# Kernel tuning notes

Measured on AMD Instinct MI355X. Metric: run time of the kernel, lower is better.

## Reference

```python
import jax, jax.numpy as jnp
import numpy as np

N_NODES = 100000
N_REL = 4
N_EDGES = 600000
D = 128


def setup_inputs() -> dict:
    key = jax.random.key(0)
    k1, k2, k3 = jax.random.split(key, 3)
    edges = jax.random.randint(k1, (N_REL, 2, N_EDGES), 0, N_NODES, dtype=jnp.int32)
    X = jax.random.normal(k2, (N_NODES, D), dtype=jnp.float32)
    # one weight matrix per relation (GraphConv weight=True, bias=False)
    W = jax.random.normal(k3, (N_REL, D, D), dtype=jnp.float32) * (1.0 / np.sqrt(D))
    return {"edges": edges, "X": X, "W": W}


def _graphconv_both(src, dst, X, W):
    # DGL GraphConv, norm='both', no bias/activation, allow_zero_in_degree.
    ones = jnp.ones((src.shape[0],), dtype=X.dtype)
    deg_out = jax.ops.segment_sum(ones, src, num_segments=N_NODES).clip(1.0)
    deg_in = jax.ops.segment_sum(ones, dst, num_segments=N_NODES).clip(1.0)
    h = X * jax.lax.rsqrt(deg_out)[:, None]          # [N, D] src-normalized
    agg = jax.ops.segment_sum(h[src], dst, num_segments=N_NODES)  # SpMM: [N, D]
    agg = agg * jax.lax.rsqrt(deg_in)[:, None]
    return agg @ W                                   # dense transform [N, D]


def reference(edges, X, W):
    # sum of per-relation GraphConv outputs (stack(...).sum(0))
    Z = jnp.zeros((N_NODES, W.shape[-1]), dtype=X.dtype)
    for r in range(N_REL):  # small fixed relation count
        Z = Z + _graphconv_both(edges[r, 0], edges[r, 1], X, W[r])
    return Z
```

## Files before the change

kernel.cpp:

```cpp
#include <hip/hip_runtime.h>
#include <hip/hip_bf16.h>

constexpr int N_NODES = 100000;
constexpr int N_REL   = 4;
constexpr int N_EDGES = 600000;
constexpr int MAXDEG  = 32;
constexpr int D       = 128;
constexpr int KTOT    = N_REL * D;
constexpr int M_PAD   = 100096;

constexpr int NB   = 128;
constexpr int BW   = 784;
constexpr int NKEY = N_REL * NB;
constexpr int CAP  = 5632;
constexpr int EPB  = 2048;
constexpr int TOT_E   = N_REL * N_EDGES;
constexpr int P1_BLKS = (TOT_E + EPB - 1) / EPB;
constexpr int XC_BLKS = (N_NODES * D / 4) / 256;
constexpr int WC_BLKS = (N_REL * D * D) / 256;

typedef __attribute__((ext_vector_type(8))) short bf16x8;
typedef __attribute__((ext_vector_type(4))) float f32x4;

static __device__ __forceinline__ unsigned short f2bf(float f) {
    union { float f; unsigned int u; } v; v.f = f;
    unsigned int r = (v.u + 0x7fffu + ((v.u >> 16) & 1u)) >> 16;
    return (unsigned short)r;
}

__global__ __launch_bounds__(256) void pass1(const int* __restrict__ edges,
                                             int* __restrict__ gcur,
                                             unsigned* __restrict__ bktd,
                                             unsigned* __restrict__ bkts,
                                             const float* __restrict__ X,
                                             unsigned short* __restrict__ Xb,
                                             const float* __restrict__ W,
                                             unsigned short* __restrict__ Wt) {
    int b = blockIdx.x;
    if (b < P1_BLKS) {
        __shared__ int hd[NKEY], hs[NKEY], bd[NKEY], bs[NKEY];
        int tid = threadIdx.x;
        for (int k = tid; k < NKEY; k += 256) { hd[k] = 0; hs[k] = 0; }
        __syncthreads();

        int e0 = b * EPB;
        int src[8], dst[8], kd[8], ks[8];
#pragma unroll
        for (int k = 0; k < 8; k++) {
            int t = e0 + k * 256 + tid;
            kd[k] = -1; ks[k] = -1; src[k] = 0; dst[k] = 0;
            if (t < TOT_E) {
                int r = t / N_EDGES;
                int e = t - r * N_EDGES;
                src[k] = edges[(size_t)(r * 2)     * N_EDGES + e];
                dst[k] = edges[(size_t)(r * 2 + 1) * N_EDGES + e];
                kd[k] = r * NB + dst[k] / BW;
                ks[k] = r * NB + src[k] / BW;
                atomicAdd(&hd[kd[k]], 1);
                atomicAdd(&hs[ks[k]], 1);
            }
        }
        __syncthreads();
        for (int k = tid; k < NKEY; k += 256) {
            int c = hd[k];
            bd[k] = c ? atomicAdd(&gcur[k * 16], c) : 0;
            hd[k] = 0;
            c = hs[k];
            bs[k] = c ? atomicAdd(&gcur[(NKEY + k) * 16], c) : 0;
            hs[k] = 0;
        }
        __syncthreads();
#pragma unroll
        for (int k = 0; k < 8; k++) {
            if (kd[k] >= 0) {
                int dstloc = dst[k] - (kd[k] - (kd[k] >> 7) * NB) * BW;
                int p = bd[kd[k]] + atomicAdd(&hd[kd[k]], 1);
                if (p < CAP) bktd[(size_t)kd[k] * CAP + p] = (unsigned)src[k] | ((unsigned)dstloc << 17);
                p = bs[ks[k]] + atomicAdd(&hs[ks[k]], 1);
                if (p < CAP) bkts[(size_t)ks[k] * CAP + p] = (unsigned)src[k];
            }
        }
    } else if (b < P1_BLKS + XC_BLKS) {
        int t = (b - P1_BLKS) * 256 + threadIdx.x;
        float4 v = ((const float4*)X)[t];
        union { unsigned short u[4]; uint2 d; } o;
        o.u[0] = f2bf(v.x); o.u[1] = f2bf(v.y); o.u[2] = f2bf(v.z); o.u[3] = f2bf(v.w);
        ((uint2*)Xb)[t] = o.d;
    } else {
        int t = (b - P1_BLKS - XC_BLKS) * 256 + threadIdx.x;
        int r = t >> 14;
        int k = (t >> 7) & 127;
        int n = t & 127;
        Wt[(size_t)n * KTOT + r * D + k] = f2bf(W[t]);
    }
}

__global__ __launch_bounds__(1024) void pass2a(const int* __restrict__ gcur,
                                               const unsigned* __restrict__ bkts,
                                               float* __restrict__ routf) {
    __shared__ int cur[BW];
    int b = blockIdx.x, tid = threadIdx.x;
    if (tid < BW) cur[tid] = 0;
    __syncthreads();
    int r = b >> 7;
    int node0 = (b & 127) * BW;
    int cnt = min(gcur[(NKEY + b) * 16], CAP);
    for (int i = tid; i < cnt; i += 1024)
        atomicAdd(&cur[(int)bkts[(size_t)b * CAP + i] - node0], 1);
    __syncthreads();
    int nN = min(BW, N_NODES - node0);
    if (tid < nN) {
        int c = cur[tid];
        routf[r * N_NODES + node0 + tid] = rsqrtf((float)(c < 1 ? 1 : c));
    }
}

__global__ __launch_bounds__(1024) void pass2b(const int* __restrict__ gcur,
                                               const unsigned* __restrict__ bktd,
                                               const float* __restrict__ routf,
                                               uint2* __restrict__ esrcc,
                                               int* __restrict__ indeg) {
    __shared__ int cur[BW];
    int b = blockIdx.x, tid = threadIdx.x;
    if (tid < BW) cur[tid] = 0;
    __syncthreads();
    int r = b >> 7;
    int node0 = (b & 127) * BW;
    int cnt = min(gcur[b * 16], CAP);
    for (int i = tid; i < cnt; i += 1024) {
        unsigned rec = bktd[(size_t)b * CAP + i];
        int s      = (int)(rec & 0x1FFFFu);
        int dstloc = (int)(rec >> 17);
        int pos = atomicAdd(&cur[dstloc], 1);
        if (pos < MAXDEG) {
            union { float f; unsigned u; } c; c.f = routf[r * N_NODES + s];
            esrcc[((size_t)r * N_NODES + node0 + dstloc) * MAXDEG + pos] = make_uint2((unsigned)s, c.u);
        }
    }
    __syncthreads();
    int nN = min(BW, N_NODES - node0);
    if (tid < nN) indeg[r * N_NODES + node0 + tid] = cur[tid];
}

__global__ __launch_bounds__(256) void gather_ell(const uint2* __restrict__ esrcc,
                                                  const int* __restrict__ indeg,
                                                  const uint2* __restrict__ Xv,
                                                  uint2* __restrict__ A2) {
    __shared__ uint2 meta[8][N_REL][MAXDEG];
    int tid = threadIdx.x;
    int h   = tid >> 5;
    int l31 = tid & 31;
    int d   = blockIdx.x * 8 + h;

    int   n[N_REL];
    float rin[N_REL];
    int nm = 0;
#pragma unroll
    for (int r = 0; r < N_REL; r++) {
        int ind = indeg[r * N_NODES + d];
        n[r]   = ind > MAXDEG ? MAXDEG : ind;
        rin[r] = rsqrtf((float)(ind < 1 ? 1 : ind));
        nm = max(nm, n[r]);
        uint2 m = make_uint2(0u, 0u);
        if (l31 < n[r])
            m = esrcc[((size_t)r * N_NODES + d) * MAXDEG + l31];
        meta[h][r][l31] = m;
    }
    int nmax = max(nm, __shfl_xor(nm, 32));
    __syncthreads();

    float4 acc[N_REL];
#pragma unroll
    for (int r = 0; r < N_REL; r++) acc[r] = make_float4(0.f, 0.f, 0.f, 0.f);

#pragma unroll 4
    for (int i = 0; i < nmax; i++) {
        uint2 m[N_REL];
#pragma unroll
        for (int r = 0; r < N_REL; r++) m[r] = meta[h][r][i];
        uint2 v[N_REL];
#pragma unroll
        for (int r = 0; r < N_REL; r++)
            v[r] = Xv[(size_t)m[r].x * (D / 4) + l31];
#pragma unroll
        for (int r = 0; r < N_REL; r++) {
            union { unsigned u; float f; } cc; cc.u = m[r].y;
            union { unsigned u; float f; } a, b, e, g;
            a.u = v[r].x << 16; b.u = v[r].x & 0xFFFF0000u;
            e.u = v[r].y << 16; g.u = v[r].y & 0xFFFF0000u;
            acc[r].x += cc.f * a.f;
            acc[r].y += cc.f * b.f;
            acc[r].z += cc.f * e.f;
            acc[r].w += cc.f * g.f;
        }
    }

#pragma unroll
    for (int r = 0; r < N_REL; r++) {
        unsigned p0 = (unsigned)f2bf(rin[r] * acc[r].x) | ((unsigned)f2bf(rin[r] * acc[r].y) << 16);
        unsigned p1 = (unsigned)f2bf(rin[r] * acc[r].z) | ((unsigned)f2bf(rin[r] * acc[r].w) << 16);
        A2[(size_t)d * (KTOT / 4) + r * (D / 4) + l31] = make_uint2(p0, p1);
    }
}

__global__ __launch_bounds__(256) void gemm_mfma(const unsigned short* __restrict__ A,
                                                 const unsigned short* __restrict__ Wt,
                                                 float* __restrict__ Z) {
    int w    = threadIdx.x >> 6;
    int lane = threadIdx.x & 63;
    int l15  = lane & 15;
    int quad = lane >> 4;
    int row0 = blockIdx.x * 128 + w * 32;

    f32x4 acc[2][8];
#pragma unroll
    for (int m = 0; m < 2; m++)
#pragma unroll
        for (int j = 0; j < 8; j++) acc[m][j] = (f32x4){0.f, 0.f, 0.f, 0.f};

    for (int k0 = 0; k0 < KTOT; k0 += 32) {
        bf16x8 a[2];
#pragma unroll
        for (int m = 0; m < 2; m++)
            a[m] = *(const bf16x8*)(A + (size_t)(row0 + m * 16 + l15) * KTOT + k0 + quad * 8);
#pragma unroll
        for (int j = 0; j < 8; j++) {
            bf16x8 b = *(const bf16x8*)(Wt + (size_t)(j * 16 + l15) * KTOT + k0 + quad * 8);
            acc[0][j] = __builtin_amdgcn_mfma_f32_16x16x32_bf16(a[0], b, acc[0][j], 0, 0, 0);
            acc[1][j] = __builtin_amdgcn_mfma_f32_16x16x32_bf16(a[1], b, acc[1][j], 0, 0, 0);
        }
    }

#pragma unroll
    for (int m = 0; m < 2; m++)
#pragma unroll
        for (int reg = 0; reg < 4; reg++) {
            int row = row0 + m * 16 + quad * 4 + reg;
            if (row < N_NODES) {
#pragma unroll
                for (int j = 0; j < 8; j++)
                    Z[(size_t)row * D + j * 16 + l15] = acc[m][j][reg];
            }
        }
}

extern "C" void kernel_launch(void* const* d_in, const int* in_sizes, int n_in,
                              void* d_out, int out_size, void* d_ws, size_t ws_size,
                              hipStream_t stream) {
    const int*   edges = (const int*)d_in[0];
    const float* X     = (const float*)d_in[1];
    const float* W     = (const float*)d_in[2];
    float*       Z     = (float*)d_out;

    auto align256 = [](size_t x) { return (x + 255) & ~(size_t)255; };
    char* ws = (char*)d_ws;
    size_t off = 0;
    int* gcur          = (int*)(ws + off);            off = align256(off + (size_t)2 * NKEY * 16 * sizeof(int));
    int* indeg         = (int*)(ws + off);            off = align256(off + (size_t)N_REL * N_NODES * sizeof(int));
    float* routf       = (float*)(ws + off);          off = align256(off + (size_t)N_REL * N_NODES * sizeof(float));
    uint2* esrcc       = (uint2*)(ws + off);          off = align256(off + (size_t)N_REL * N_NODES * MAXDEG * sizeof(uint2));
    unsigned short* Xb = (unsigned short*)(ws + off); off = align256(off + (size_t)N_NODES * D * sizeof(short));
    unsigned short* Wt = (unsigned short*)(ws + off); off = align256(off + (size_t)KTOT * D * sizeof(short));
    unsigned short* A  = (unsigned short*)(ws + off); off = align256(off + (size_t)M_PAD * KTOT * sizeof(short));
    unsigned* bktd = (unsigned*)A;
    unsigned* bkts = (unsigned*)((char*)A + (size_t)NKEY * CAP * sizeof(unsigned));

    hipMemsetAsync(gcur, 0, (size_t)2 * NKEY * 16 * sizeof(int), stream);

    pass1<<<P1_BLKS + XC_BLKS + WC_BLKS, 256, 0, stream>>>(
        edges, gcur, bktd, bkts, X, Xb, W, Wt);

    pass2a<<<NKEY, 1024, 0, stream>>>(gcur, bkts, routf);

    pass2b<<<NKEY, 1024, 0, stream>>>(gcur, bktd, routf, esrcc, indeg);

    gather_ell<<<N_NODES / 8, 256, 0, stream>>>(
        esrcc, indeg, (const uint2*)Xb, (uint2*)A);

    gemm_mfma<<<M_PAD / 128, 256, 0, stream>>>(A, Wt, Z);
}
```

Before: 363.6 us.

## Fuse ELL gather aggregation with MFMA GEMM via swizzled shared-memory tile

Merges the gather kernel and the GEMM kernel into one. Each block aggregates 32 destination nodes for all relations into an XOR-swizzled bf16 LDS tile, then runs the 32x512 by 512x128 MFMA product directly from shared memory. This removes the write and reread of the 100K x 512 bf16 intermediate A in global memory and one kernel launch. The cost is 32KB of LDS per block, which lowers occupancy for the latency-bound gather phase, and W tiles are now reloaded by many more, smaller blocks.

After: 378.1 us. 1.04x slower.

```diff
diff --git a/kernel.cpp b/kernel.cpp
--- a/kernel.cpp
+++ b/kernel.cpp
@@ -7,7 +7,6 @@
 constexpr int MAXDEG  = 32;
 constexpr int D       = 128;
 constexpr int KTOT    = N_REL * D;
-constexpr int M_PAD   = 100096;
 
 constexpr int NB   = 128;
 constexpr int BW   = 784;
@@ -142,106 +141,109 @@
     if (tid < nN) indeg[r * N_NODES + node0 + tid] = cur[tid];
 }
 
-__global__ __launch_bounds__(256) void gather_ell(const uint2* __restrict__ esrcc,
-                                                  const int* __restrict__ indeg,
-                                                  const uint2* __restrict__ Xv,
-                                                  uint2* __restrict__ A2) {
+__global__ __launch_bounds__(256) void gather_gemm(const uint2* __restrict__ esrcc,
+                                                   const int* __restrict__ indeg,
+                                                   const uint2* __restrict__ Xv,
+                                                   const unsigned short* __restrict__ Wt,
+                                                   float* __restrict__ Z) {
+    __shared__ unsigned short Atile[32][512];
     __shared__ uint2 meta[8][N_REL][MAXDEG];
-    int tid = threadIdx.x;
-    int h   = tid >> 5;
-    int l31 = tid & 31;
-    int d   = blockIdx.x * 8 + h;
-
-    int   n[N_REL];
-    float rin[N_REL];
-    int nm = 0;
-#pragma unroll
-    for (int r = 0; r < N_REL; r++) {
-        int ind = indeg[r * N_NODES + d];
-        n[r]   = ind > MAXDEG ? MAXDEG : ind;
-        rin[r] = rsqrtf((float)(ind < 1 ? 1 : ind));
-        nm = max(nm, n[r]);
-        uint2 m = make_uint2(0u, 0u);
-        if (l31 < n[r])
-            m = esrcc[((size_t)r * N_NODES + d) * MAXDEG + l31];
-        meta[h][r][l31] = m;
-    }
-    int nmax = max(nm, __shfl_xor(nm, 32));
-    __syncthreads();
-
-    float4 acc[N_REL];
-#pragma unroll
-    for (int r = 0; r < N_REL; r++) acc[r] = make_float4(0.f, 0.f, 0.f, 0.f);
+
+    int tid   = threadIdx.x;
+    int h     = tid >> 5;
+    int l31   = tid & 31;
+    int node0 = blockIdx.x * 32;
+
+    for (int sub = 0; sub < 4; sub++) {
+        int node = sub * 8 + h;
+        int d    = node0 + node;
+
+        int   n[N_REL];
+        float rin[N_REL];
+        int nm = 0;
+#pragma unroll
+        for (int r = 0; r < N_REL; r++) {
+            int ind = indeg[r * N_NODES + d];
+            n[r]   = ind > MAXDEG ? MAXDEG : ind;
+            rin[r] = rsqrtf((float)(ind < 1 ? 1 : ind));
+            nm = max(nm, n[r]);
+            uint2 m = make_uint2(0u, 0u);
+            if (l31 < n[r])
+                m = esrcc[((size_t)r * N_NODES + d) * MAXDEG + l31];
+            meta[h][r][l31] = m;
+        }
+        int nmax = max(nm, __shfl_xor(nm, 32));
+
+        float4 acc[N_REL];
+#pragma unroll
+        for (int r = 0; r < N_REL; r++) acc[r] = make_float4(0.f, 0.f, 0.f, 0.f);
 
 #pragma unroll 4
-    for (int i = 0; i < nmax; i++) {
-        uint2 m[N_REL];
-#pragma unroll
-        for (int r = 0; r < N_REL; r++) m[r] = meta[h][r][i];
-        uint2 v[N_REL];
-#pragma unroll
-        for (int r = 0; r < N_REL; r++)
-            v[r] = Xv[(size_t)m[r].x * (D / 4) + l31];
+        for (int i = 0; i < nmax; i++) {
+            uint2 m[N_REL];
+#pragma unroll
+            for (int r = 0; r < N_REL; r++) m[r] = meta[h][r][i];
+            uint2 v[N_REL];
+#pragma unroll
+            for (int r = 0; r < N_REL; r++)
+                v[r] = Xv[(size_t)m[r].x * (D / 4) + l31];
+#pragma unroll
+            for (int r = 0; r < N_REL; r++) {
+                union { unsigned u; float f; } cc; cc.u = m[r].y;
+                union { unsigned u; float f; } a, b, e, g;
+                a.u = v[r].x << 16; b.u = v[r].x & 0xFFFF0000u;
+                e.u = v[r].y << 16; g.u = v[r].y & 0xFFFF0000u;
+                acc[r].x += cc.f * a.f;
+                acc[r].y += cc.f * b.f;
+                acc[r].z += cc.f * e.f;
+                acc[r].w += cc.f * g.f;
+            }
+        }
+
+        unsigned sw = (unsigned)((node & 7) << 4);
 #pragma unroll
         for (int r = 0; r < N_REL; r++) {
-            union { unsigned u; float f; } cc; cc.u = m[r].y;
-            union { unsigned u; float f; } a, b, e, g;
-            a.u = v[r].x << 16; b.u = v[r].x & 0xFFFF0000u;
-            e.u = v[r].y << 16; g.u = v[r].y & 0xFFFF0000u;
-            acc[r].x += cc.f * a.f;
-            acc[r].y += cc.f * b.f;
-            acc[r].z += cc.f * e.f;
-            acc[r].w += cc.f * g.f;
-        }
-    }
-
-#pragma unroll
-    for (int r = 0; r < N_REL; r++) {
-        unsigned p0 = (unsigned)f2bf(rin[r] * acc[r].x) | ((unsigned)f2bf(rin[r] * acc[r].y) << 16);
-        unsigned p1 = (unsigned)f2bf(rin[r] * acc[r].z) | ((unsigned)f2bf(rin[r] * acc[r].w) << 16);
-        A2[(size_t)d * (KTOT / 4) + r * (D / 4) + l31] = make_uint2(p0, p1);
-    }
-}
-
-__global__ __launch_bounds__(256) void gemm_mfma(const unsigned short* __restrict__ A,
-                                                 const unsigned short* __restrict__ Wt,
-                                                 float* __restrict__ Z) {
-    int w    = threadIdx.x >> 6;
-    int lane = threadIdx.x & 63;
+            unsigned p0 = (unsigned)f2bf(rin[r] * acc[r].x) | ((unsigned)f2bf(rin[r] * acc[r].y) << 16);
+            unsigned p1 = (unsigned)f2bf(rin[r] * acc[r].z) | ((unsigned)f2bf(rin[r] * acc[r].w) << 16);
+            unsigned off = (unsigned)node * 1024u + (((unsigned)(r * 32 + l31) * 8u) ^ sw);
+            *(uint2*)((char*)Atile + off) = make_uint2(p0, p1);
+        }
+    }
+    __syncthreads();
+
+    int w    = tid >> 6;
+    int lane = tid & 63;
     int l15  = lane & 15;
     int quad = lane >> 4;
-    int row0 = blockIdx.x * 128 + w * 32;
-
-    f32x4 acc[2][8];
-#pragma unroll
-    for (int m = 0; m < 2; m++)
-#pragma unroll
-        for (int j = 0; j < 8; j++) acc[m][j] = (f32x4){0.f, 0.f, 0.f, 0.f};
-
+    int m    = w >> 1;
+    int half = w & 1;
+
+    f32x4 acc[4];
+#pragma unroll
+    for (int n = 0; n < 4; n++) acc[n] = (f32x4){0.f, 0.f, 0.f, 0.f};
+
+    int arow = m * 16 + l15;
+    unsigned asw = (unsigned)((arow & 7) << 4);
     for (int k0 = 0; k0 < KTOT; k0 += 32) {
-        bf16x8 a[2];
-#pragma unroll
-        for (int m = 0; m < 2; m++)
-            a[m] = *(const bf16x8*)(A + (size_t)(row0 + m * 16 + l15) * KTOT + k0 + quad * 8);
-#pragma unroll
-        for (int j = 0; j < 8; j++) {
+        unsigned aoff = (unsigned)arow * 1024u + (((unsigned)(k0 + quad * 8) * 2u) ^ asw);
+        bf16x8 a = *(const bf16x8*)((const char*)Atile + aoff);
+#pragma unroll
+        for (int n = 0; n < 4; n++) {
+            int j = half * 4 + n;
             bf16x8 b = *(const bf16x8*)(Wt + (size_t)(j * 16 + l15) * KTOT + k0 + quad * 8);
-            acc[0][j] = __builtin_amdgcn_mfma_f32_16x16x32_bf16(a[0], b, acc[0][j], 0, 0, 0);
-            acc[1][j] = __builtin_amdgcn_mfma_f32_16x16x32_bf16(a[1], b, acc[1][j], 0, 0, 0);
-        }
-    }
-
-#pragma unroll
-    for (int m = 0; m < 2; m++)
+            acc[n] = __builtin_amdgcn_mfma_f32_16x16x32_bf16(a, b, acc[n], 0, 0, 0);
+        }
+    }
+
+#pragma unroll
+    for (int n = 0; n < 4; n++) {
+        int j = half * 4 + n;
 #pragma unroll
         for (int reg = 0; reg < 4; reg++) {
-            int row = row0 + m * 16 + quad * 4 + reg;
-            if (row < N_NODES) {
-#pragma unroll
-                for (int j = 0; j < 8; j++)
-                    Z[(size_t)row * D + j * 16 + l15] = acc[m][j][reg];
-            }
-        }
+            int row = node0 + m * 16 + quad * 4 + reg;
+            Z[(size_t)row * D + j * 16 + l15] = acc[n][reg];
+        }
+    }
 }
 
 extern "C" void kernel_launch(void* const* d_in, const int* in_sizes, int n_in,
@@ -261,9 +263,8 @@
     uint2* esrcc       = (uint2*)(ws + off);          off = align256(off + (size_t)N_REL * N_NODES * MAXDEG * sizeof(uint2));
     unsigned short* Xb = (unsigned short*)(ws + off); off = align256(off + (size_t)N_NODES * D * sizeof(short));
     unsigned short* Wt = (unsigned short*)(ws + off); off = align256(off + (size_t)KTOT * D * sizeof(short));
-    unsigned short* A  = (unsigned short*)(ws + off); off = align256(off + (size_t)M_PAD * KTOT * sizeof(short));
-    unsigned* bktd = (unsigned*)A;
-    unsigned* bkts = (unsigned*)((char*)A + (size_t)NKEY * CAP * sizeof(unsigned));
+    unsigned* bktd     = (unsigned*)(ws + off);       off = align256(off + (size_t)NKEY * CAP * sizeof(unsigned));
+    unsigned* bkts     = (unsigned*)(ws + off);       off = align256(off + (size_t)NKEY * CAP * sizeof(unsigned));
 
     hipMemsetAsync(gcur, 0, (size_t)2 * NKEY * 16 * sizeof(int), stream);
 
@@ -274,8 +275,6 @@
 
     pass2b<<<NKEY, 1024, 0, stream>>>(gcur, bktd, routf, esrcc, indeg);
 
-    gather_ell<<<N_NODES / 8, 256, 0, stream>>>(
-        esrcc, indeg, (const uint2*)Xb, (uint2*)A);
-
-    gemm_mfma<<<M_PAD / 128, 256, 0, stream>>>(A, Wt, Z);
-}
+    gather_gemm<<<N_NODES / 32, 256, 0, stream>>>(
+        esrcc, indeg, (const uint2*)Xb, Wt, Z);
+}
```

## Locally sort edges by bucket in LDS before coalesced bucket scatter

Applied to the files above, without the earlier changes.

The edge bucketing pass now builds a per-block counting sort in shared memory. Each block ranks its edges per bucket, takes an exclusive prefix sum, places the packed records contiguously in LDS, and then writes each bucket's run to global memory in order. The aim is to replace scattered per-edge global writes with mostly contiguous runs that coalesce better. The block size doubles to 4096 edges, and the dst and src sides are now processed one after the other. This adds shared-memory traffic, more barriers, and a second read of the src indices.

Result: no change. 366.7 us (+0.9%).

```diff
diff --git a/kernel.cpp b/kernel.cpp
--- a/kernel.cpp
+++ b/kernel.cpp
@@ -13,9 +13,9 @@
 constexpr int BW   = 784;
 constexpr int NKEY = N_REL * NB;
 constexpr int CAP  = 5632;
-constexpr int EPB  = 2048;
+constexpr int EPB1 = 4096;
 constexpr int TOT_E   = N_REL * N_EDGES;
-constexpr int P1_BLKS = (TOT_E + EPB - 1) / EPB;
+constexpr int B1_BLKS = (TOT_E + EPB1 - 1) / EPB1;
 constexpr int XC_BLKS = (N_NODES * D / 4) / 256;
 constexpr int WC_BLKS = (N_REL * D * D) / 256;
 
@@ -37,57 +37,107 @@
                                              const float* __restrict__ W,
                                              unsigned short* __restrict__ Wt) {
     int b = blockIdx.x;
-    if (b < P1_BLKS) {
-        __shared__ int hd[NKEY], hs[NKEY], bd[NKEY], bs[NKEY];
-        int tid = threadIdx.x;
-        for (int k = tid; k < NKEY; k += 256) { hd[k] = 0; hs[k] = 0; }
-        __syncthreads();
-
-        int e0 = b * EPB;
-        int src[8], dst[8], kd[8], ks[8];
-#pragma unroll
-        for (int k = 0; k < 8; k++) {
-            int t = e0 + k * 256 + tid;
-            kd[k] = -1; ks[k] = -1; src[k] = 0; dst[k] = 0;
-            if (t < TOT_E) {
-                int r = t / N_EDGES;
-                int e = t - r * N_EDGES;
-                src[k] = edges[(size_t)(r * 2)     * N_EDGES + e];
-                dst[k] = edges[(size_t)(r * 2 + 1) * N_EDGES + e];
-                kd[k] = r * NB + dst[k] / BW;
-                ks[k] = r * NB + src[k] / BW;
-                atomicAdd(&hd[kd[k]], 1);
-                atomicAdd(&hs[ks[k]], 1);
-            }
-        }
-        __syncthreads();
-        for (int k = tid; k < NKEY; k += 256) {
-            int c = hd[k];
-            bd[k] = c ? atomicAdd(&gcur[k * 16], c) : 0;
-            hd[k] = 0;
-            c = hs[k];
-            bs[k] = c ? atomicAdd(&gcur[(NKEY + k) * 16], c) : 0;
-            hs[k] = 0;
-        }
-        __syncthreads();
-#pragma unroll
-        for (int k = 0; k < 8; k++) {
-            if (kd[k] >= 0) {
-                int dstloc = dst[k] - (kd[k] - (kd[k] >> 7) * NB) * BW;
-                int p = bd[kd[k]] + atomicAdd(&hd[kd[k]], 1);
-                if (p < CAP) bktd[(size_t)kd[k] * CAP + p] = (unsigned)src[k] | ((unsigned)dstloc << 17);
-                p = bs[ks[k]] + atomicAdd(&hs[ks[k]], 1);
-                if (p < CAP) bkts[(size_t)ks[k] * CAP + p] = (unsigned)src[k];
-            }
-        }
-    } else if (b < P1_BLKS + XC_BLKS) {
-        int t = (b - P1_BLKS) * 256 + threadIdx.x;
+    if (b < B1_BLKS) {
+        __shared__ unsigned kr[EPB1];
+        __shared__ unsigned sorted[EPB1];
+        __shared__ unsigned short keyp[EPB1];
+        __shared__ int h[NKEY], gb[NKEY], pfx[NKEY + 1];
+        __shared__ int wsum[4];
+        int tid  = threadIdx.x;
+        int lane = tid & 63, wv = tid >> 6;
+        int e0   = b * EPB1;
+        int nval = min(EPB1, TOT_E - e0);
+
+        for (int side = 0; side < 2; side++) {
+            for (int k = tid; k < NKEY; k += 256) h[k] = 0;
+            __syncthreads();
+            for (int i = tid; i < EPB1; i += 256) {
+                unsigned v = 0xFFFFFFFFu;
+                if (i < nval) {
+                    int t = e0 + i;
+                    int r = t / N_EDGES, e = t - r * N_EDGES;
+                    if (side == 0) {
+                        int dst = edges[(size_t)(r * 2 + 1) * N_EDGES + e];
+                        int bkt = dst / BW;
+                        int dstloc = dst - bkt * BW;
+                        int rank = atomicAdd(&h[r * NB + bkt], 1);
+                        v = ((unsigned)bkt << 22) | ((unsigned)dstloc << 12) | (unsigned)rank;
+                    } else {
+                        int src = edges[(size_t)(r * 2) * N_EDGES + e];
+                        int bkt = src / BW;
+                        int rank = atomicAdd(&h[r * NB + bkt], 1);
+                        v = ((unsigned)src << 12) | (unsigned)rank;
+                    }
+                }
+                kr[i] = v;
+            }
+            __syncthreads();
+            for (int k = tid; k < NKEY; k += 256) {
+                int c = h[k];
+                gb[k] = c ? atomicAdd(&gcur[(side * NKEY + k) * 16], c) : 0;
+            }
+            int a0 = h[2 * tid], a1 = h[2 * tid + 1];
+            int s  = a0 + a1;
+            int incl = s;
+#pragma unroll
+            for (int dlt = 1; dlt < 64; dlt <<= 1) {
+                int n = __shfl_up(incl, dlt);
+                if (lane >= dlt) incl += n;
+            }
+            if (lane == 63) wsum[wv] = incl;
+            __syncthreads();
+            int woff = 0;
+            for (int wwi = 0; wwi < wv; wwi++) woff += wsum[wwi];
+            int excl = incl - s + woff;
+            pfx[2 * tid]     = excl;
+            pfx[2 * tid + 1] = excl + a0;
+            if (tid == 255) pfx[NKEY] = excl + s;
+            __syncthreads();
+            for (int i = tid; i < EPB1; i += 256) {
+                unsigned v = kr[i];
+                if (v != 0xFFFFFFFFu) {
+                    int t = e0 + i;
+                    int r = t / N_EDGES;
+                    int key, pos;
+                    unsigned rec;
+                    if (side == 0) {
+                        int e   = t - r * N_EDGES;
+                        int src = edges[(size_t)(r * 2) * N_EDGES + e];
+                        int bkt    = (int)(v >> 22);
+                        int dstloc = (int)((v >> 12) & 0x3FFu);
+                        key = r * NB + bkt;
+                        pos = pfx[key] + (int)(v & 0xFFFu);
+                        rec = (unsigned)src | ((unsigned)dstloc << 17);
+                    } else {
+                        int src = (int)(v >> 12);
+                        key = r * NB + src / BW;
+                        pos = pfx[key] + (int)(v & 0xFFFu);
+                        rec = (unsigned)src;
+                    }
+                    sorted[pos] = rec;
+                    keyp[pos]   = (unsigned short)key;
+                }
+            }
+            __syncthreads();
+            {
+                unsigned* out = side == 0 ? bktd : bkts;
+                int tot = pfx[NKEY];
+                for (int j = tid; j < tot; j += 256) {
+                    int k   = keyp[j];
+                    int idx = gb[k] + (j - pfx[k]);
+                    if (idx < CAP) out[(size_t)k * CAP + idx] = sorted[j];
+                }
+            }
+            __syncthreads();
+        }
+    } else if (b < B1_BLKS + XC_BLKS) {
+        int t = (b - B1_BLKS) * 256 + threadIdx.x;
         float4 v = ((const float4*)X)[t];
         union { unsigned short u[4]; uint2 d; } o;
         o.u[0] = f2bf(v.x); o.u[1] = f2bf(v.y); o.u[2] = f2bf(v.z); o.u[3] = f2bf(v.w);
         ((uint2*)Xb)[t] = o.d;
     } else {
-        int t = (b - P1_BLKS - XC_BLKS) * 256 + threadIdx.x;
+        int t = (b - B1_BLKS - XC_BLKS) * 256 + threadIdx.x;
         int r = t >> 14;
         int k = (t >> 7) & 127;
         int n = t & 127;
@@ -267,7 +317,7 @@
 
     hipMemsetAsync(gcur, 0, (size_t)2 * NKEY * 16 * sizeof(int), stream);
 
-    pass1<<<P1_BLKS + XC_BLKS + WC_BLKS, 256, 0, stream>>>(
+    pass1<<<B1_BLKS + XC_BLKS + WC_BLKS, 256, 0, stream>>>(
         edges, gcur, bktd, bkts, X, Xb, W, Wt);
 
     pass2a<<<NKEY, 1024, 0, stream>>>(gcur, bkts, routf);
```
